# Performance work log

Measured on AMD Instinct MI355X. Metric: run time of the kernel, lower is better.

The kernel has to match this reference:

```python
import jax, jax.numpy as jnp
import numpy as np

BATCH, SEQ, DIM = 4, 4096, 256
DT_RANK, D_STATE, NUM_TOKENS = 16, 16, 1024


def _adapool(x, T):
    # uniform window mean == AdaptiveAvgPool1d when S % T == 0
    B, S, D = x.shape
    return x.reshape(B, T, S // T, D).mean(axis=2)


def _layernorm(x, g, b, eps=1e-5):
    mu = x.mean(-1, keepdims=True)
    var = ((x - mu) ** 2).mean(-1, keepdims=True)
    return (x - mu) * jax.lax.rsqrt(var + eps) * g + b


def _gauss_mask(T):
    c = (T + 1) // 2
    idx = jnp.arange(T, dtype=jnp.float32)
    sigma = jnp.abs(idx - c).mean()
    w = jnp.exp(-0.5 * (idx - c) ** 2 / sigma ** 2)
    return w / w.sum()


def _ssm(x, Wdbc, Wdt, bdt, Alog, D):
    A = -jnp.exp(Alog)                                     # (Dm, N)
    dbc = x @ Wdbc.T                                       # (B,L,dt+2N)
    delta = jax.nn.softplus(dbc[..., :DT_RANK] @ Wdt.T + bdt)   # (B,L,Dm)
    Bm = dbc[..., DT_RANK:DT_RANK + D_STATE]               # (B,L,N)
    Cm = dbc[..., DT_RANK + D_STATE:]                      # (B,L,N)
    deltaA = jnp.exp(delta[..., None] * A)                 # (B,L,Dm,N)
    BX = (delta[..., None] * Bm[:, :, None, :]) * x[..., None]
    def comb(c1, c2):
        a1, x1 = c1
        a2, x2 = c2
        return (a2 * a1, a2 * x1 + x2)
    _, hs = jax.lax.associative_scan(comb, (deltaA, BX), axis=1)
    y = jnp.einsum('bldn,bln->bld', hs, Cm) + D * x
    return y


def setup_inputs():
    key = jax.random.key(0)
    ks = jax.random.split(key, 16)
    s = 0.05
    Alog = jnp.tile(jnp.log(jnp.arange(1.0, D_STATE + 1.0, dtype=jnp.float32))[None, :], (DIM, 1))
    return {
        'x': jax.random.normal(ks[0], (BATCH, SEQ, DIM), jnp.float32),
        'ln_g': jnp.ones((DIM,), jnp.float32),
        'ln_b': jnp.zeros((DIM,), jnp.float32),
        'W1': jax.random.normal(ks[1], (DIM, DIM), jnp.float32) * s,
        'b1': jnp.zeros((DIM,), jnp.float32),
        'W2': jax.random.normal(ks[2], (DIM, DIM), jnp.float32) * s,
        'b2': jnp.zeros((DIM,), jnp.float32),
        'Wcf': jax.random.normal(ks[3], (DIM, DIM), jnp.float32) * s,
        'bcf': jnp.zeros((DIM,), jnp.float32),
        'Wcb': jax.random.normal(ks[4], (DIM, DIM), jnp.float32) * s,
        'bcb': jnp.zeros((DIM,), jnp.float32),
        'Wdbc_f': jax.random.normal(ks[5], (DT_RANK + 2 * D_STATE, DIM), jnp.float32) * s,
        'Wdt_f': jax.random.normal(ks[6], (DIM, DT_RANK), jnp.float32) * s,
        'bdt_f': jnp.zeros((DIM,), jnp.float32),
        'Alog_f': Alog,
        'D_f': jnp.ones((DIM,), jnp.float32),
        'Wdbc_b': jax.random.normal(ks[7], (DT_RANK + 2 * D_STATE, DIM), jnp.float32) * s,
        'Wdt_b': jax.random.normal(ks[8], (DIM, DT_RANK), jnp.float32) * s,
        'bdt_b': jnp.zeros((DIM,), jnp.float32),
        'Alog_b': Alog,
        'D_b': jnp.ones((DIM,), jnp.float32),
    }


def reference(x, ln_g, ln_b, W1, b1, W2, b2, Wcf, bcf, Wcb, bcb,
              Wdbc_f, Wdt_f, bdt_f, Alog_f, D_f,
              Wdbc_b, Wdt_b, bdt_b, Alog_b, D_b):
    skip = _adapool(x, NUM_TOKENS)
    xn = _layernorm(x, ln_g, ln_b)
    z = xn @ W1.T + b1
    xp = xn @ W2.T + b2
    mask = _gauss_mask(NUM_TOKENS)[None, :, None]

    # forward direction: 1x1 conv (= channel linear) -> softplus -> SSM
    h1 = jax.nn.softplus(jnp.einsum('bsd,ed->bse', xp, Wcf) + bcf)
    x1 = _ssm(h1, Wdbc_f, Wdt_f, bdt_f, Alog_f, D_f)
    x1 = jax.nn.silu(_adapool(x1, NUM_TOKENS) * mask)

    # backward direction on flipped sequence
    h2 = jax.nn.softplus(jnp.einsum('bsd,ed->bse', xp[:, ::-1], Wcb) + bcb)
    x2 = _ssm(h2, Wdbc_b, Wdt_b, bdt_b, Alog_b, D_b)[:, ::-1]
    x2 = jax.nn.silu(_adapool(x2, NUM_TOKENS) * mask)

    zp = jax.nn.silu(_adapool(z, NUM_TOKENS))
    return zp * x1 + zp * x2 + skip
```

## Files before the change

kernel.cpp:

```cpp
#include <hip/hip_runtime.h>
#include <math.h>


namespace {
constexpr int BB = 4;
constexpr int LL = 4096;
constexpr int DD = 256;
constexpr int NS = 16;
constexpr int NCH = 64;
constexpr int CLEN = 64;
constexpr int TOK = 1024;

constexpr size_t NROW = (size_t)BB * LL;
constexpr size_t NE   = NROW * DD;
constexpr size_t NP   = (size_t)BB * TOK * DD;
constexpr size_t NBC  = NROW * NS;
constexpr size_t NAGG = 2ull * BB * DD * NCH * NS;

constexpr size_t O_H1X  = 0;
constexpr size_t O_G2X  = NE / 2;
constexpr size_t O_H1T  = NE;
constexpr size_t O_G2T  = NE + NE / 2;
constexpr size_t O_DLTF = 2 * NE;
constexpr size_t O_XN   = O_DLTF;
constexpr size_t O_DLTB = 2 * NE + NE / 2;
constexpr size_t O_BMF  = 3 * NE;
constexpr size_t O_CMF  = O_BMF + NBC / 2;
constexpr size_t O_BMB  = O_CMF + NBC / 2;
constexpr size_t O_CMB  = O_BMB + NBC / 2;
constexpr size_t O_ZP   = O_CMB + NBC / 2;
constexpr size_t O_SKIP = O_ZP + NP;
constexpr size_t O_Y1   = O_SKIP + NP;
constexpr size_t O_Y2   = O_Y1 + NP;
constexpr size_t O_WF1  = O_Y2 + NP;
constexpr size_t O_BF1  = O_WF1 + 768 * 256 / 2;
constexpr size_t O_WF2F = O_BF1 + 768;
constexpr size_t O_B2F  = O_WF2F + 384 * 256 / 2;
constexpr size_t O_WF2B = O_B2F + 384;
constexpr size_t O_B2B  = O_WF2B + 384 * 256 / 2;
constexpr size_t O_APROD = O_B2B + 384;
constexpr size_t O_HEND = O_APROD + NAGG;
constexpr size_t O_HIN  = O_HEND + NAGG;
constexpr size_t O_MASK = O_HIN + NAGG;

constexpr int SST = 136;
}

typedef __bf16 bf16x8 __attribute__((ext_vector_type(8)));
typedef __bf16 bf16x4 __attribute__((ext_vector_type(4)));
typedef float f32x4 __attribute__((ext_vector_type(4)));

__device__ __forceinline__ float softplusf(float x) {
    return fmaxf(x, 0.f) + __logf(1.f + __expf(-fabsf(x)));
}
__device__ __forceinline__ float siluf(float x) {
    return x / (1.f + __expf(-x));
}
__device__ __forceinline__ void gl_lds16(const void* g, void* l) {
    __builtin_amdgcn_global_load_lds((const __attribute__((address_space(1))) unsigned int*)g,
                                     (__attribute__((address_space(3))) unsigned int*)l, 16, 0, 0);
}
__device__ __forceinline__ int st_addr(int col, int row) {
    return col * SST + ((((row >> 3) ^ (col >> 3)) & 15) << 3) + (row & 7);
}
__device__ __forceinline__ void pow_chain(float e1, float* p) {
    p[0] = e1;
    p[1] = e1 * e1;
    p[2] = p[1] * e1;
    p[3] = p[1] * p[1];
    p[4] = p[3] * p[0];
    p[5] = p[3] * p[1];
    p[6] = p[3] * p[2];
    p[7] = p[3] * p[3];
    p[8]  = p[7] * p[0];
    p[9]  = p[7] * p[1];
    p[10] = p[7] * p[2];
    p[11] = p[7] * p[3];
    p[12] = p[7] * p[4];
    p[13] = p[7] * p[5];
    p[14] = p[7] * p[6];
    p[15] = p[7] * p[7];
}

__global__ __launch_bounds__(256) void prep_all_kernel(
    const float* __restrict__ W1, const float* __restrict__ b1,
    const float* __restrict__ W2, const float* __restrict__ b2,
    const float* __restrict__ Wcf, const float* __restrict__ bcf,
    const float* __restrict__ Wcb, const float* __restrict__ bcb,
    const float* __restrict__ Wdt_f, const float* __restrict__ Wdbc_f, const float* __restrict__ bdt_f,
    const float* __restrict__ Wdt_b, const float* __restrict__ Wdbc_b, const float* __restrict__ bdt_b,
    __bf16* __restrict__ Wf1, float* __restrict__ bf1,
    __bf16* __restrict__ Wf2f, float* __restrict__ b2f,
    __bf16* __restrict__ Wf2b, float* __restrict__ b2b,
    float* __restrict__ mask)
{
    int bx = blockIdx.x, mat = blockIdx.y, k = threadIdx.x;
    if (bx < 256) {
        int j = bx;
        const float* Wc = mat ? Wcb : Wcf;
        float acc = 0.f, accb = 0.f;
#pragma unroll 8
        for (int m = 0; m < 256; ++m) {
            float w = Wc[j * 256 + m];
            acc  = fmaf(w, W2[m * 256 + k], acc);
            accb = fmaf(w, b2[m], accb);
        }
        Wf1[(size_t)(256 + mat * 256 + j) * 256 + k] = (__bf16)acc;
        if (k == 0) bf1[256 + mat * 256 + j] = accb + (mat ? bcb[j] : bcf[j]);
        if (mat == 0) {
            Wf1[(size_t)j * 256 + k] = (__bf16)W1[j * 256 + k];
            if (k == 0) bf1[j] = b1[j];
        }
    } else if (bx < 640) {
        int j = bx - 256;
        const float* Wdt  = mat ? Wdt_b : Wdt_f;
        const float* Wdbc = mat ? Wdbc_b : Wdbc_f;
        const float* bdt  = mat ? bdt_b : bdt_f;
        __bf16* Wf2 = mat ? Wf2b : Wf2f;
        float* b2x  = mat ? b2b : b2f;
        float val;
        if (j < 256) {
            float acc = 0.f;
#pragma unroll
            for (int m = 0; m < 16; ++m)
                acc = fmaf(Wdt[j * 16 + m], Wdbc[m * 256 + k], acc);
            val = acc;
        } else if (j < 288) {
            val = Wdbc[(16 + (j - 256)) * 256 + k];
        } else {
            val = 0.f;
        }
        Wf2[(size_t)j * 256 + k] = (__bf16)val;
        if (k == 0) b2x[j] = (j < 256) ? bdt[j] : 0.f;
    } else if (mat == 0) {
        __shared__ float red[4];
        __shared__ float sb;
        float w[4];
        float loc = 0.f;
#pragma unroll
        for (int q = 0; q < 4; ++q) {
            float dd = (float)(k + 256 * q) - 512.f;
            w[q] = __expf(-0.5f * dd * dd * (1.f / 65536.f));
            loc += w[q];
        }
        for (int o = 32; o > 0; o >>= 1) loc += __shfl_xor(loc, o, 64);
        if ((k & 63) == 0) red[k >> 6] = loc;
        __syncthreads();
        if (k == 0) sb = red[0] + red[1] + red[2] + red[3];
        __syncthreads();
        float inv = 1.f / sb;
#pragma unroll
        for (int q = 0; q < 4; ++q) mask[k + 256 * q] = w[q] * inv;
    }
}

__global__ __launch_bounds__(256) void ln_kernel(
    const float* __restrict__ x, const float* __restrict__ lng, const float* __restrict__ lnb,
    __bf16* __restrict__ xn, float* __restrict__ skipo)
{
    __shared__ float red[32];
    __shared__ float mv[8];
    int t = threadIdx.x;
    int r0 = blockIdx.x * 4;
    float gg = lng[t], bbv = lnb[t];
    float v[4], s[4], q[4];
#pragma unroll
    for (int i = 0; i < 4; ++i) {
        v[i] = x[(size_t)(r0 + i) * 256 + t];
        s[i] = v[i];
        q[i] = v[i] * v[i];
    }
    for (int o = 32; o > 0; o >>= 1) {
#pragma unroll
        for (int i = 0; i < 4; ++i) {
            s[i] += __shfl_xor(s[i], o, 64);
            q[i] += __shfl_xor(q[i], o, 64);
        }
    }
    if ((t & 63) == 0) {
        int w = t >> 6;
#pragma unroll
        for (int i = 0; i < 4; ++i) { red[i * 4 + w] = s[i]; red[16 + i * 4 + w] = q[i]; }
    }
    __syncthreads();
    if (t < 4) {
        float S = red[t * 4 + 0] + red[t * 4 + 1] + red[t * 4 + 2] + red[t * 4 + 3];
        float Q = red[16 + t * 4 + 0] + red[16 + t * 4 + 1] + red[16 + t * 4 + 2] + red[16 + t * 4 + 3];
        float mu = S * (1.f / 256.f);
        mv[t * 2] = mu;
        mv[t * 2 + 1] = rsqrtf(Q * (1.f / 256.f) - mu * mu + 1e-5f);
    }
    __syncthreads();
    float acc = 0.f;
#pragma unroll
    for (int i = 0; i < 4; ++i) {
        xn[(size_t)(r0 + i) * 256 + t] = (__bf16)((v[i] - mv[i * 2]) * mv[i * 2 + 1] * gg + bbv);
        acc += v[i];
    }
    int b = r0 >> 12;
    int g = (r0 & 4095) >> 2;
    skipo[((size_t)b * TOK + g) * 256 + t] = acc * 0.25f;
}

__global__ __launch_bounds__(256) void gemm1_mfma(
    const __bf16* __restrict__ A, const __bf16* __restrict__ Bw, const float* __restrict__ bias,
    float* __restrict__ zp, __bf16* __restrict__ h1x, __bf16* __restrict__ g2x,
    __bf16* __restrict__ h1T, __bf16* __restrict__ g2T)
{
    __shared__ __align__(16) __bf16 SH[128 * SST];
    __bf16* As = SH;
    __bf16* Bs = SH + 4096;
    int tid = threadIdx.x;
    int lane = tid & 63, wv = tid >> 6;
    int wr = wv >> 1, wc = wv & 1;
    int lm = lane & 15, lq = lane >> 4;
    int m0 = blockIdx.x << 7, n0 = blockIdx.y << 7;

    const __bf16* ga0 = A  + (size_t)(m0 + wv * 32 + lm) * 256 + lq * 8;
    const __bf16* ga1 = ga0 + 16 * 256;
    const __bf16* gb0 = Bw + (size_t)(n0 + wv * 32 + lm) * 256 + lq * 8;
    const __bf16* gb1 = gb0 + 16 * 256;
    __bf16* la0 = &As[(wv * 2    ) * 512];
    __bf16* la1 = &As[(wv * 2 + 1) * 512];
    __bf16* lb0 = &Bs[(wv * 2    ) * 512];
    __bf16* lb1 = &Bs[(wv * 2 + 1) * 512];

    f32x4 acc[4][4];
#pragma unroll
    for (int i = 0; i < 4; ++i)
#pragma unroll
        for (int j = 0; j < 4; ++j) acc[i][j] = 0;

    for (int k0 = 0; k0 < 256; k0 += 32) {
        __syncthreads();
        gl_lds16(ga0 + k0, la0);
        gl_lds16(ga1 + k0, la1);
        gl_lds16(gb0 + k0, lb0);
        gl_lds16(gb1 + k0, lb1);
        __syncthreads();
        bf16x8 af[4], bfr[4];
#pragma unroll
        for (int i = 0; i < 4; ++i)
            af[i] = *(const bf16x8*)&As[(wr * 4 + i) * 512 + lane * 8];
#pragma unroll
        for (int j = 0; j < 4; ++j)
            bfr[j] = *(const bf16x8*)&Bs[(wc * 4 + j) * 512 + lane * 8];
#pragma unroll
        for (int i = 0; i < 4; ++i)
#pragma unroll
            for (int j = 0; j < 4; ++j)
                acc[i][j] = __builtin_amdgcn_mfma_f32_16x16x32_bf16(af[i], bfr[j], acc[i][j], 0, 0, 0);
    }

    int target = blockIdx.y >> 1;
    int colbase = (blockIdx.y & 1) * 128;
    __syncthreads();
    if (target == 0) {
        float* zs = (float*)SH;
#pragma unroll
        for (int j = 0; j < 4; ++j) {
            int coll = wc * 64 + j * 16 + lm;
            float bv = bias[n0 + coll];
#pragma unroll
            for (int i = 0; i < 4; ++i) {
                int gl = wr * 16 + i * 4 + lq;
                float s = acc[i][j][0] + acc[i][j][1] + acc[i][j][2] + acc[i][j][3];
                zs[gl * 132 + coll] = siluf(0.25f * s + bv);
            }
        }
        __syncthreads();
        int b = m0 >> 12, g0 = (m0 & 4095) >> 2;
        int rl = tid >> 5;
        int c4 = (tid & 31) * 4;
#pragma unroll
        for (int p = 0; p < 4; ++p) {
            int g = p * 8 + rl;
            float4 v = *(float4*)&zs[g * 132 + c4];
            *(float4*)&zp[((size_t)b * TOK + g0 + g) * 256 + colbase + c4] = v;
        }
    } else {
        __bf16* hs = SH;
#pragma unroll
        for (int j = 0; j < 4; ++j) {
            int coll = wc * 64 + j * 16 + lm;
            float bv = bias[n0 + coll];
#pragma unroll
            for (int i = 0; i < 4; ++i) {
                int rl = wr * 64 + i * 16 + lq * 4;
                bf16x4 v4;
#pragma unroll
                for (int r = 0; r < 4; ++r)
                    v4[r] = (__bf16)softplusf(acc[i][j][r] + bv);
                *(bf16x4*)&hs[st_addr(coll, rl)] = v4;
            }
        }
        __syncthreads();
        __bf16* outp = (target == 1) ? h1x : g2x;
        __bf16* outT = (target == 1) ? h1T : g2T;
        {
            int tg = tid & 15;
#pragma unroll
            for (int it = 0; it < 8; ++it) {
                int dl_ = it * 16 + (tid >> 4);
                bf16x8 v = *(const bf16x8*)&hs[dl_ * SST + (((tg ^ (dl_ >> 3)) & 15) << 3)];
                *(bf16x8*)&outT[(size_t)(colbase + dl_) * 16384 + m0 + tg * 8] = v;
            }
        }
        {
            int rl2 = tid >> 4;
            int c8 = (tid & 15) * 8;
#pragma unroll
            for (int p = 0; p < 8; ++p) {
                int row = p * 16 + rl2;
                bf16x8 v;
#pragma unroll
                for (int e = 0; e < 8; ++e) v[e] = hs[st_addr(c8 + e, row)];
                *(bf16x8*)&outp[(size_t)(m0 + row) * 256 + colbase + c8] = v;
            }
        }
    }
}

__global__ __launch_bounds__(256) void gemm2_mfma(
    const __bf16* __restrict__ h1x, const __bf16* __restrict__ g2x,
    const __bf16* __restrict__ Wf, const float* __restrict__ bf2,
    const __bf16* __restrict__ Wb, const float* __restrict__ bb2,
    __bf16* __restrict__ dTf, __bf16* __restrict__ dTb,
    __bf16* __restrict__ BmF, __bf16* __restrict__ CmF,
    __bf16* __restrict__ BmB, __bf16* __restrict__ CmB)
{
    __shared__ __align__(16) __bf16 SH[128 * SST];
    __bf16* As = SH;
    __bf16* Bs = SH + 4096;
    int tid = threadIdx.x;
    int lane = tid & 63, wv = tid >> 6;
    int wr = wv >> 1, wc = wv & 1;
    int lm = lane & 15, lq = lane >> 4;
    int m0 = blockIdx.x << 7, n0 = blockIdx.y << 7;
    int dir = blockIdx.z;
    const __bf16* A    = dir ? g2x : h1x;
    const __bf16* Bw   = dir ? Wb : Wf;
    const float* bias  = dir ? bb2 : bf2;
    __bf16* dT = dir ? dTb : dTf;
    __bf16* Bm = dir ? BmB : BmF;
    __bf16* Cm = dir ? CmB : CmF;

    const __bf16* ga0 = A  + (size_t)(m0 + wv * 32 + lm) * 256 + lq * 8;
    const __bf16* ga1 = ga0 + 16 * 256;
    const __bf16* gb0 = Bw + (size_t)(n0 + wv * 32 + lm) * 256 + lq * 8;
    const __bf16* gb1 = gb0 + 16 * 256;
    __bf16* la0 = &As[(wv * 2    ) * 512];
    __bf16* la1 = &As[(wv * 2 + 1) * 512];
    __bf16* lb0 = &Bs[(wv * 2    ) * 512];
    __bf16* lb1 = &Bs[(wv * 2 + 1) * 512];

    f32x4 acc[4][4];
#pragma unroll
    for (int i = 0; i < 4; ++i)
#pragma unroll
        for (int j = 0; j < 4; ++j) acc[i][j] = 0;

    for (int k0 = 0; k0 < 256; k0 += 32) {
        __syncthreads();
        gl_lds16(ga0 + k0, la0);
        gl_lds16(ga1 + k0, la1);
        gl_lds16(gb0 + k0, lb0);
        gl_lds16(gb1 + k0, lb1);
        __syncthreads();
        bf16x8 af[4], bfr[4];
#pragma unroll
        for (int i = 0; i < 4; ++i)
            af[i] = *(const bf16x8*)&As[(wr * 4 + i) * 512 + lane * 8];
#pragma unroll
        for (int j = 0; j < 4; ++j)
            bfr[j] = *(const bf16x8*)&Bs[(wc * 4 + j) * 512 + lane * 8];
#pragma unroll
        for (int i = 0; i < 4; ++i)
#pragma unroll
            for (int j = 0; j < 4; ++j)
                acc[i][j] = __builtin_amdgcn_mfma_f32_16x16x32_bf16(af[i], bfr[j], acc[i][j], 0, 0, 0);
    }

    __syncthreads();
    if (blockIdx.y < 2) {
        __bf16* hs = SH;
        int colbase = blockIdx.y * 128;
#pragma unroll
        for (int j = 0; j < 4; ++j) {
            int coll = wc * 64 + j * 16 + lm;
            float bv = bias[n0 + coll];
#pragma unroll
            for (int i = 0; i < 4; ++i) {
                int rl = wr * 64 + i * 16 + lq * 4;
                bf16x4 v4;
#pragma unroll
                for (int r = 0; r < 4; ++r)
                    v4[r] = (__bf16)softplusf(acc[i][j][r] + bv);
                *(bf16x4*)&hs[st_addr(coll, rl)] = v4;
            }
        }
        __syncthreads();
        int tg = tid & 15;
#pragma unroll
        for (int it = 0; it < 8; ++it) {
            int dl_ = it * 16 + (tid >> 4);
            bf16x8 v = *(const bf16x8*)&hs[dl_ * SST + (((tg ^ (dl_ >> 3)) & 15) << 3)];
            *(bf16x8*)&dT[(size_t)(colbase + dl_) * 16384 + m0 + tg * 8] = v;
        }
    } else {
        __bf16* bs_ = SH;
        __bf16* cs_ = SH + 128 * 24;
        if (wc == 0) {
#pragma unroll
            for (int j = 0; j < 2; ++j) {
                int coll = j * 16 + lm;
                float bv = bias[n0 + coll];
                __bf16* dst = j ? cs_ : bs_;
#pragma unroll
                for (int i = 0; i < 4; ++i) {
                    int rl = wr * 64 + i * 16 + lq * 4;
#pragma unroll
                    for (int r = 0; r < 4; ++r)
                        dst[(rl + r) * 24 + lm] = (__bf16)(acc[i][j][r] + bv);
                }
            }
        }
        __syncthreads();
        int row = tid >> 1;
        int c8 = (tid & 1) * 8;
        bf16x8 vb = *(bf16x8*)&bs_[row * 24 + c8];
        bf16x8 vc = *(bf16x8*)&cs_[row * 24 + c8];
        *(bf16x8*)&Bm[(size_t)(m0 + row) * 16 + c8] = vb;
        *(bf16x8*)&Cm[(size_t)(m0 + row) * 16 + c8] = vc;
    }
}

__global__ __launch_bounds__(256) void scan1_kernel(
    const __bf16* __restrict__ dTf, const __bf16* __restrict__ dTb,
    const __bf16* __restrict__ xTf, const __bf16* __restrict__ xTb,
    const __bf16* __restrict__ bmf, const __bf16* __restrict__ bmb,
    const float* __restrict__ alogf, const float* __restrict__ alogb,
    float* __restrict__ aprod, float* __restrict__ hend)
{
    int d = threadIdx.x;
    int c = blockIdx.x, b = blockIdx.y, dir = blockIdx.z;
    const __bf16* dT = dir ? dTb : dTf;
    const __bf16* xT = dir ? xTb : xTf;
    const __bf16* Bm = dir ? bmb : bmf;
    const float* Alog = dir ? alogb : alogf;

    float A[16];
    bool intOK = true;
#pragma unroll
    for (int n = 0; n < 16; ++n) {
        A[n] = -__expf(Alog[(size_t)d * 16 + n]);
        intOK = intOK && (fabsf(A[n] + (float)(n + 1)) < 1e-3f);
    }
    float h[16];
#pragma unroll
    for (int n = 0; n < 16; ++n) h[n] = 0.f;
    float sd = 0.f;
    size_t tb = (size_t)d * 16384 + (size_t)b * 4096 + (size_t)c * CLEN;
    size_t rowb = (size_t)b * LL + (size_t)c * CLEN;
    if (intOK) {
        for (int g = 0; g < 8; ++g) {
            int tblk = dir ? (56 - 8 * g) : 8 * g;
            bf16x8 dv = *(const bf16x8*)&dT[tb + tblk];
            bf16x8 xv8 = *(const bf16x8*)&xT[tb + tblk];
#pragma unroll
            for (int ii = 0; ii < 8; ++ii) {
                int i = dir ? (7 - ii) : ii;
                float dlt = (float)dv[i];
                float xv  = (float)xv8[i];
                float common = dlt * xv;
                sd += dlt;
                float p[16];
                pow_chain(__expf(-dlt), p);
                const bf16x8* Bp = (const bf16x8*)&Bm[(rowb + tblk + i) * NS];
                bf16x8 b0 = Bp[0], b1 = Bp[1];
#pragma unroll
                for (int n = 0; n < 8; ++n) {
                    h[n]     = fmaf(p[n],     h[n],     common * (float)b0[n]);
                    h[n + 8] = fmaf(p[n + 8], h[n + 8], common * (float)b1[n]);
                }
            }
        }
        float pe[16];
        pow_chain(__expf(-sd), pe);
        size_t idx = ((((size_t)dir * BB + b) * DD + d) * NCH + c) * NS;
#pragma unroll
        for (int q = 0; q < 4; ++q) {
            float4 av, hv;
            av.x = pe[q * 4 + 0]; av.y = pe[q * 4 + 1]; av.z = pe[q * 4 + 2]; av.w = pe[q * 4 + 3];
            hv.x = h[q * 4 + 0];  hv.y = h[q * 4 + 1];  hv.z = h[q * 4 + 2];  hv.w = h[q * 4 + 3];
            *(float4*)&aprod[idx + q * 4] = av;
            *(float4*)&hend[idx + q * 4] = hv;
        }
    } else {
        for (int g = 0; g < 8; ++g) {
            int tblk = dir ? (56 - 8 * g) : 8 * g;
            bf16x8 dv = *(const bf16x8*)&dT[tb + tblk];
            bf16x8 xv8 = *(const bf16x8*)&xT[tb + tblk];
#pragma unroll
            for (int ii = 0; ii < 8; ++ii) {
                int i = dir ? (7 - ii) : ii;
                float dlt = (float)dv[i];
                float xv  = (float)xv8[i];
                float common = dlt * xv;
                sd += dlt;
                const bf16x8* Bp = (const bf16x8*)&Bm[(rowb + tblk + i) * NS];
                bf16x8 b0 = Bp[0], b1 = Bp[1];
#pragma unroll
                for (int n = 0; n < 8; ++n) {
                    h[n]     = fmaf(__expf(dlt * A[n]),     h[n],     common * (float)b0[n]);
                    h[n + 8] = fmaf(__expf(dlt * A[n + 8]), h[n + 8], common * (float)b1[n]);
                }
            }
        }
        size_t idx = ((((size_t)dir * BB + b) * DD + d) * NCH + c) * NS;
#pragma unroll
        for (int n = 0; n < 16; ++n) {
            aprod[idx + n] = __expf(sd * A[n]);
            hend[idx + n] = h[n];
        }
    }
}

__global__ __launch_bounds__(256) void scan2_kernel(
    const float* __restrict__ aprod, const float* __restrict__ hend,
    float* __restrict__ hin)
{
    int g = blockIdx.x * 256 + threadIdx.x;
    int n = g & 15, d = (g >> 4) & 255, b = (g >> 12) & 3, dir = (g >> 14) & 1;
    size_t bidx = (((size_t)dir * BB + b) * DD + d) * NCH;
    float s = 0.f;
    if (!dir) {
#pragma unroll 8
        for (int c = 0; c < NCH; ++c) {
            size_t idx = (bidx + c) * NS + n;
            hin[idx] = s;
            s = fmaf(aprod[idx], s, hend[idx]);
        }
    } else {
#pragma unroll 8
        for (int c = NCH - 1; c >= 0; --c) {
            size_t idx = (bidx + c) * NS + n;
            hin[idx] = s;
            s = fmaf(aprod[idx], s, hend[idx]);
        }
    }
}

__global__ __launch_bounds__(256) void scan3_kernel(
    const __bf16* __restrict__ dTf, const __bf16* __restrict__ dTb,
    const __bf16* __restrict__ xTf, const __bf16* __restrict__ xTb,
    const __bf16* __restrict__ bmf, const __bf16* __restrict__ bmb,
    const __bf16* __restrict__ cmf, const __bf16* __restrict__ cmb,
    const float* __restrict__ alogf, const float* __restrict__ alogb,
    const float* __restrict__ Dfp, const float* __restrict__ Dbp,
    const float* __restrict__ hin,
    float* __restrict__ y1, float* __restrict__ y2)
{
    int d = threadIdx.x;
    int c = blockIdx.x, b = blockIdx.y, dir = blockIdx.z;
    const __bf16* dT = dir ? dTb : dTf;
    const __bf16* xT = dir ? xTb : xTf;
    const __bf16* Bm = dir ? bmb : bmf;
    const __bf16* Cm = dir ? cmb : cmf;
    const float* Alog = dir ? alogb : alogf;
    const float* Dv   = dir ? Dbp : Dfp;
    float* yout = dir ? y2 : y1;

    float A[16];
    bool intOK = true;
#pragma unroll
    for (int n = 0; n < 16; ++n) {
        A[n] = -__expf(Alog[(size_t)d * 16 + n]);
        intOK = intOK && (fabsf(A[n] + (float)(n + 1)) < 1e-3f);
    }
    float Dd = Dv[d];
    float h[16];
    size_t idx = ((((size_t)dir * BB + b) * DD + d) * NCH + c) * NS;
#pragma unroll
    for (int q = 0; q < 4; ++q) {
        float4 hv = *(const float4*)&hin[idx + q * 4];
        h[q * 4 + 0] = hv.x; h[q * 4 + 1] = hv.y; h[q * 4 + 2] = hv.z; h[q * 4 + 3] = hv.w;
    }
    size_t tb = (size_t)d * 16384 + (size_t)b * 4096 + (size_t)c * CLEN;
    size_t rowb = (size_t)b * LL + (size_t)c * CLEN;
    int base = c * CLEN;
    float pool = 0.f;
    if (intOK) {
        for (int g = 0; g < 8; ++g) {
            int tblk = dir ? (56 - 8 * g) : 8 * g;
            bf16x8 dv = *(const bf16x8*)&dT[tb + tblk];
            bf16x8 xv8 = *(const bf16x8*)&xT[tb + tblk];
#pragma unroll
            for (int ii = 0; ii < 8; ++ii) {
                int i = dir ? (7 - ii) : ii;
                float dlt = (float)dv[i];
                float xv  = (float)xv8[i];
                float common = dlt * xv;
                float p[16];
                pow_chain(__expf(-dlt), p);
                const bf16x8* Bp = (const bf16x8*)&Bm[(rowb + tblk + i) * NS];
                const bf16x8* Cp = (const bf16x8*)&Cm[(rowb + tblk + i) * NS];
                bf16x8 b0 = Bp[0], b1 = Bp[1];
                bf16x8 c0 = Cp[0], c1 = Cp[1];
                float yac = 0.f;
#pragma unroll
                for (int n = 0; n < 8; ++n) {
                    h[n]     = fmaf(p[n],     h[n],     common * (float)b0[n]);
                    h[n + 8] = fmaf(p[n + 8], h[n + 8], common * (float)b1[n]);
                    yac = fmaf(h[n], (float)c0[n], yac);
                    yac = fmaf(h[n + 8], (float)c1[n], yac);
                }
                pool += yac + Dd * xv;
                int t = base + tblk + i;
                bool gend = dir ? ((t & 3) == 0) : ((t & 3) == 3);
                if (gend) {
                    yout[((size_t)b * TOK + (t >> 2)) * DD + d] = pool * 0.25f;
                    pool = 0.f;
                }
            }
        }
    } else {
        for (int g = 0; g < 8; ++g) {
            int tblk = dir ? (56 - 8 * g) : 8 * g;
            bf16x8 dv = *(const bf16x8*)&dT[tb + tblk];
            bf16x8 xv8 = *(const bf16x8*)&xT[tb + tblk];
#pragma unroll
            for (int ii = 0; ii < 8; ++ii) {
                int i = dir ? (7 - ii) : ii;
                float dlt = (float)dv[i];
                float xv  = (float)xv8[i];
                float common = dlt * xv;
                const bf16x8* Bp = (const bf16x8*)&Bm[(rowb + tblk + i) * NS];
                const bf16x8* Cp = (const bf16x8*)&Cm[(rowb + tblk + i) * NS];
                bf16x8 b0 = Bp[0], b1 = Bp[1];
                bf16x8 c0 = Cp[0], c1 = Cp[1];
                float yac = 0.f;
#pragma unroll
                for (int n = 0; n < 8; ++n) {
                    h[n]     = fmaf(__expf(dlt * A[n]),     h[n],     common * (float)b0[n]);
                    h[n + 8] = fmaf(__expf(dlt * A[n + 8]), h[n + 8], common * (float)b1[n]);
                    yac = fmaf(h[n], (float)c0[n], yac);
                    yac = fmaf(h[n + 8], (float)c1[n], yac);
                }
                pool += yac + Dd * xv;
                int t = base + tblk + i;
                bool gend = dir ? ((t & 3) == 0) : ((t & 3) == 3);
                if (gend) {
                    yout[((size_t)b * TOK + (t >> 2)) * DD + d] = pool * 0.25f;
                    pool = 0.f;
                }
            }
        }
    }
}

__global__ __launch_bounds__(256) void final_kernel(
    const float* __restrict__ zp, const float* __restrict__ y1, const float* __restrict__ y2,
    const float* __restrict__ mask, const float* __restrict__ skipi, float* __restrict__ out)
{
    int p = blockIdx.x;
    int g = p & 1023;
    int d = threadIdx.x;
    size_t ip = (size_t)p * 256 + d;
    float mk = mask[g];
    float a1 = y1[ip] * mk, a2 = y2[ip] * mk;
    out[ip] = zp[ip] * (siluf(a1) + siluf(a2)) + skipi[ip];
}

extern "C" void kernel_launch(void* const* d_in, const int* in_sizes, int n_in,
                              void* d_out, int out_size, void* d_ws, size_t ws_size,
                              hipStream_t stream)
{
    const float* x      = (const float*)d_in[0];
    const float* ln_g   = (const float*)d_in[1];
    const float* ln_b   = (const float*)d_in[2];
    const float* W1     = (const float*)d_in[3];
    const float* b1     = (const float*)d_in[4];
    const float* W2     = (const float*)d_in[5];
    const float* b2     = (const float*)d_in[6];
    const float* Wcf    = (const float*)d_in[7];
    const float* bcf    = (const float*)d_in[8];
    const float* Wcb    = (const float*)d_in[9];
    const float* bcb    = (const float*)d_in[10];
    const float* Wdbc_f = (const float*)d_in[11];
    const float* Wdt_f  = (const float*)d_in[12];
    const float* bdt_f  = (const float*)d_in[13];
    const float* Alog_f = (const float*)d_in[14];
    const float* D_f    = (const float*)d_in[15];
    const float* Wdbc_b = (const float*)d_in[16];
    const float* Wdt_b  = (const float*)d_in[17];
    const float* bdt_b  = (const float*)d_in[18];
    const float* Alog_b = (const float*)d_in[19];
    const float* D_b    = (const float*)d_in[20];
    float* out = (float*)d_out;
    float* ws  = (float*)d_ws;

    __bf16* h1x = (__bf16*)(ws + O_H1X);
    __bf16* g2x = (__bf16*)(ws + O_G2X);
    __bf16* h1T = (__bf16*)(ws + O_H1T);
    __bf16* g2T = (__bf16*)(ws + O_G2T);
    __bf16* xnb = (__bf16*)(ws + O_XN);
    __bf16* dTf = (__bf16*)(ws + O_DLTF);
    __bf16* dTb = (__bf16*)(ws + O_DLTB);
    __bf16* bmf = (__bf16*)(ws + O_BMF);
    __bf16* cmf = (__bf16*)(ws + O_CMF);
    __bf16* bmb = (__bf16*)(ws + O_BMB);
    __bf16* cmb = (__bf16*)(ws + O_CMB);
    float* zpb  = ws + O_ZP;
    float* skb  = ws + O_SKIP;
    float* y1b  = ws + O_Y1;
    float* y2b  = ws + O_Y2;
    __bf16* wf1 = (__bf16*)(ws + O_WF1);
    float* bf1  = ws + O_BF1;
    __bf16* wf2f = (__bf16*)(ws + O_WF2F);
    float* b2f  = ws + O_B2F;
    __bf16* wf2b = (__bf16*)(ws + O_WF2B);
    float* b2b  = ws + O_B2B;
    float* apr  = ws + O_APROD;
    float* hnd  = ws + O_HEND;
    float* hin  = ws + O_HIN;
    float* mkb  = ws + O_MASK;

    prep_all_kernel<<<dim3(641, 2), 256, 0, stream>>>(
        W1, b1, W2, b2, Wcf, bcf, Wcb, bcb,
        Wdt_f, Wdbc_f, bdt_f, Wdt_b, Wdbc_b, bdt_b,
        wf1, bf1, wf2f, b2f, wf2b, b2b, mkb);
    ln_kernel<<<4096, 256, 0, stream>>>(x, ln_g, ln_b, xnb, skb);
    gemm1_mfma<<<dim3(128, 6), 256, 0, stream>>>(xnb, wf1, bf1, zpb, h1x, g2x, h1T, g2T);
    gemm2_mfma<<<dim3(128, 3, 2), 256, 0, stream>>>(h1x, g2x, wf2f, b2f, wf2b, b2b,
                                                    dTf, dTb, bmf, cmf, bmb, cmb);
    scan1_kernel<<<dim3(NCH, BB, 2), 256, 0, stream>>>(dTf, dTb, h1T, g2T, bmf, bmb,
                                                       Alog_f, Alog_b, apr, hnd);
    scan2_kernel<<<128, 256, 0, stream>>>(apr, hnd, hin);
    scan3_kernel<<<dim3(NCH, BB, 2), 256, 0, stream>>>(dTf, dTb, h1T, g2T, bmf, bmb, cmf, cmb,
                                                       Alog_f, Alog_b, D_f, D_b, hin, y1b, y2b);
    final_kernel<<<4096, 256, 0, stream>>>(zpb, y1b, y2b, mkb, skb, out);
}
```

Measured before the change: 249.9 us.

## Interleave transposed delta/x in 8-step groups and store chunk sums instead of decay products

Changes the transposed delta and activation buffers from a per-channel contiguous layout (stride 16384) to groups of 8 timesteps interleaved across channels. Adjacent threads in the scan kernels now read adjacent 16-byte vectors, which coalesces those loads. The chunk summaries become [chunk][n][d] with d innermost, and scan1 stores only the summed delta per chunk rather than 16 decay products. scan2 recomputes exp(sd*A) from that sum, cutting summary traffic at the cost of extra exp work in the small serial pass.

```diff
diff --git a/kernel.cpp b/kernel.cpp
--- a/kernel.cpp
+++ b/kernel.cpp
@@ -16,6 +16,7 @@
 constexpr size_t NP   = (size_t)BB * TOK * DD;
 constexpr size_t NBC  = NROW * NS;
 constexpr size_t NAGG = 2ull * BB * DD * NCH * NS;
+constexpr size_t NSD  = 2ull * BB * NCH * DD;
 
 constexpr size_t O_H1X  = 0;
 constexpr size_t O_G2X  = NE / 2;
@@ -38,8 +39,8 @@
 constexpr size_t O_B2F  = O_WF2F + 384 * 256 / 2;
 constexpr size_t O_WF2B = O_B2F + 384;
 constexpr size_t O_B2B  = O_WF2B + 384 * 256 / 2;
-constexpr size_t O_APROD = O_B2B + 384;
-constexpr size_t O_HEND = O_APROD + NAGG;
+constexpr size_t O_SD   = O_B2B + 384;
+constexpr size_t O_HEND = O_SD + NSD;
 constexpr size_t O_HIN  = O_HEND + NAGG;
 constexpr size_t O_MASK = O_HIN + NAGG;
 
@@ -298,12 +299,12 @@
         __bf16* outp = (target == 1) ? h1x : g2x;
         __bf16* outT = (target == 1) ? h1T : g2T;
         {
-            int tg = tid & 15;
+            int tg = tid >> 4;
 #pragma unroll
             for (int it = 0; it < 8; ++it) {
-                int dl_ = it * 16 + (tid >> 4);
-                bf16x8 v = *(const bf16x8*)&hs[dl_ * SST + (((tg ^ (dl_ >> 3)) & 15) << 3)];
-                *(bf16x8*)&outT[(size_t)(colbase + dl_) * 16384 + m0 + tg * 8] = v;
+                int dcol = it * 16 + (tid & 15);
+                bf16x8 v = *(const bf16x8*)&hs[dcol * SST + (((tg ^ (dcol >> 3)) & 15) << 3)];
+                *(bf16x8*)&outT[(((size_t)(m0 >> 3) + tg) * 256 + colbase + dcol) * 8] = v;
             }
         }
         {
@@ -400,12 +401,12 @@
             }
         }
         __syncthreads();
-        int tg = tid & 15;
+        int tg = tid >> 4;
 #pragma unroll
         for (int it = 0; it < 8; ++it) {
-            int dl_ = it * 16 + (tid >> 4);
-            bf16x8 v = *(const bf16x8*)&hs[dl_ * SST + (((tg ^ (dl_ >> 3)) & 15) << 3)];
-            *(bf16x8*)&dT[(size_t)(colbase + dl_) * 16384 + m0 + tg * 8] = v;
+            int dcol = it * 16 + (tid & 15);
+            bf16x8 v = *(const bf16x8*)&hs[dcol * SST + (((tg ^ (dcol >> 3)) & 15) << 3)];
+            *(bf16x8*)&dT[(((size_t)(m0 >> 3) + tg) * 256 + colbase + dcol) * 8] = v;
         }
     } else {
         __bf16* bs_ = SH;
@@ -440,7 +441,7 @@
     const __bf16* __restrict__ xTf, const __bf16* __restrict__ xTb,
     const __bf16* __restrict__ bmf, const __bf16* __restrict__ bmb,
     const float* __restrict__ alogf, const float* __restrict__ alogb,
-    float* __restrict__ aprod, float* __restrict__ hend)
+    float* __restrict__ sdb, float* __restrict__ hend)
 {
     int d = threadIdx.x;
     int c = blockIdx.x, b = blockIdx.y, dir = blockIdx.z;
@@ -460,13 +461,14 @@
 #pragma unroll
     for (int n = 0; n < 16; ++n) h[n] = 0.f;
     float sd = 0.f;
-    size_t tb = (size_t)d * 16384 + (size_t)b * 4096 + (size_t)c * CLEN;
+    size_t rg0 = (size_t)b * 512 + (size_t)c * 8;
     size_t rowb = (size_t)b * LL + (size_t)c * CLEN;
     if (intOK) {
         for (int g = 0; g < 8; ++g) {
-            int tblk = dir ? (56 - 8 * g) : 8 * g;
-            bf16x8 dv = *(const bf16x8*)&dT[tb + tblk];
-            bf16x8 xv8 = *(const bf16x8*)&xT[tb + tblk];
+            int gg = dir ? (7 - g) : g;
+            size_t ti = ((rg0 + gg) * 256 + d) * 8;
+            bf16x8 dv = *(const bf16x8*)&dT[ti];
+            bf16x8 xv8 = *(const bf16x8*)&xT[ti];
 #pragma unroll
             for (int ii = 0; ii < 8; ++ii) {
                 int i = dir ? (7 - ii) : ii;
@@ -476,7 +478,7 @@
                 sd += dlt;
                 float p[16];
                 pow_chain(__expf(-dlt), p);
-                const bf16x8* Bp = (const bf16x8*)&Bm[(rowb + tblk + i) * NS];
+                const bf16x8* Bp = (const bf16x8*)&Bm[(rowb + gg * 8 + i) * NS];
                 bf16x8 b0 = Bp[0], b1 = Bp[1];
 #pragma unroll
                 for (int n = 0; n < 8; ++n) {
@@ -485,22 +487,12 @@
                 }
             }
         }
-        float pe[16];
-        pow_chain(__expf(-sd), pe);
-        size_t idx = ((((size_t)dir * BB + b) * DD + d) * NCH + c) * NS;
-#pragma unroll
-        for (int q = 0; q < 4; ++q) {
-            float4 av, hv;
-            av.x = pe[q * 4 + 0]; av.y = pe[q * 4 + 1]; av.z = pe[q * 4 + 2]; av.w = pe[q * 4 + 3];
-            hv.x = h[q * 4 + 0];  hv.y = h[q * 4 + 1];  hv.z = h[q * 4 + 2];  hv.w = h[q * 4 + 3];
-            *(float4*)&aprod[idx + q * 4] = av;
-            *(float4*)&hend[idx + q * 4] = hv;
-        }
     } else {
         for (int g = 0; g < 8; ++g) {
-            int tblk = dir ? (56 - 8 * g) : 8 * g;
-            bf16x8 dv = *(const bf16x8*)&dT[tb + tblk];
-            bf16x8 xv8 = *(const bf16x8*)&xT[tb + tblk];
+            int gg = dir ? (7 - g) : g;
+            size_t ti = ((rg0 + gg) * 256 + d) * 8;
+            bf16x8 dv = *(const bf16x8*)&dT[ti];
+            bf16x8 xv8 = *(const bf16x8*)&xT[ti];
 #pragma unroll
             for (int ii = 0; ii < 8; ++ii) {
                 int i = dir ? (7 - ii) : ii;
@@ -508,7 +500,7 @@
                 float xv  = (float)xv8[i];
                 float common = dlt * xv;
                 sd += dlt;
-                const bf16x8* Bp = (const bf16x8*)&Bm[(rowb + tblk + i) * NS];
+                const bf16x8* Bp = (const bf16x8*)&Bm[(rowb + gg * 8 + i) * NS];
                 bf16x8 b0 = Bp[0], b1 = Bp[1];
 #pragma unroll
                 for (int n = 0; n < 8; ++n) {
@@ -517,36 +509,43 @@
                 }
             }
         }
-        size_t idx = ((((size_t)dir * BB + b) * DD + d) * NCH + c) * NS;
-#pragma unroll
-        for (int n = 0; n < 16; ++n) {
-            aprod[idx + n] = __expf(sd * A[n]);
-            hend[idx + n] = h[n];
-        }
-    }
+    }
+    size_t sbase = (size_t)(dir * 4 + b) * NCH + c;
+    sdb[sbase * 256 + d] = sd;
+    size_t hb = sbase * 16 * 256 + d;
+#pragma unroll
+    for (int n = 0; n < 16; ++n) hend[hb + (size_t)n * 256] = h[n];
 }
 
 __global__ __launch_bounds__(256) void scan2_kernel(
-    const float* __restrict__ aprod, const float* __restrict__ hend,
+    const float* __restrict__ sdb, const float* __restrict__ hend,
+    const float* __restrict__ alogf, const float* __restrict__ alogb,
     float* __restrict__ hin)
 {
-    int g = blockIdx.x * 256 + threadIdx.x;
-    int n = g & 15, d = (g >> 4) & 255, b = (g >> 12) & 3, dir = (g >> 14) & 1;
-    size_t bidx = (((size_t)dir * BB + b) * DD + d) * NCH;
+    int blk = blockIdx.x;
+    int n = blk & 15, b = (blk >> 4) & 3, dir = blk >> 6;
+    int d = threadIdx.x;
+    const float* Alog = dir ? alogb : alogf;
+    float A_dn = -__expf(Alog[(size_t)d * 16 + n]);
+    size_t basec = (size_t)(dir * 4 + b) * NCH;
     float s = 0.f;
     if (!dir) {
 #pragma unroll 8
         for (int c = 0; c < NCH; ++c) {
-            size_t idx = (bidx + c) * NS + n;
+            float sdv = sdb[(basec + c) * 256 + d];
+            size_t idx = ((basec + c) * 16 + n) * 256 + d;
+            float he = hend[idx];
             hin[idx] = s;
-            s = fmaf(aprod[idx], s, hend[idx]);
+            s = fmaf(__expf(sdv * A_dn), s, he);
         }
     } else {
 #pragma unroll 8
         for (int c = NCH - 1; c >= 0; --c) {
-            size_t idx = (bidx + c) * NS + n;
+            float sdv = sdb[(basec + c) * 256 + d];
+            size_t idx = ((basec + c) * 16 + n) * 256 + d;
+            float he = hend[idx];
             hin[idx] = s;
-            s = fmaf(aprod[idx], s, hend[idx]);
+            s = fmaf(__expf(sdv * A_dn), s, he);
         }
     }
 }
@@ -580,21 +579,20 @@
     }
     float Dd = Dv[d];
     float h[16];
-    size_t idx = ((((size_t)dir * BB + b) * DD + d) * NCH + c) * NS;
-#pragma unroll
-    for (int q = 0; q < 4; ++q) {
-        float4 hv = *(const float4*)&hin[idx + q * 4];
-        h[q * 4 + 0] = hv.x; h[q * 4 + 1] = hv.y; h[q * 4 + 2] = hv.z; h[q * 4 + 3] = hv.w;
-    }
-    size_t tb = (size_t)d * 16384 + (size_t)b * 4096 + (size_t)c * CLEN;
+    size_t hb = ((size_t)(dir * 4 + b) * NCH + c) * 16 * 256 + d;
+#pragma unroll
+    for (int n = 0; n < 16; ++n) h[n] = hin[hb + (size_t)n * 256];
+
+    size_t rg0 = (size_t)b * 512 + (size_t)c * 8;
     size_t rowb = (size_t)b * LL + (size_t)c * CLEN;
     int base = c * CLEN;
     float pool = 0.f;
     if (intOK) {
         for (int g = 0; g < 8; ++g) {
-            int tblk = dir ? (56 - 8 * g) : 8 * g;
-            bf16x8 dv = *(const bf16x8*)&dT[tb + tblk];
-            bf16x8 xv8 = *(const bf16x8*)&xT[tb + tblk];
+            int gg = dir ? (7 - g) : g;
+            size_t ti = ((rg0 + gg) * 256 + d) * 8;
+            bf16x8 dv = *(const bf16x8*)&dT[ti];
+            bf16x8 xv8 = *(const bf16x8*)&xT[ti];
 #pragma unroll
             for (int ii = 0; ii < 8; ++ii) {
                 int i = dir ? (7 - ii) : ii;
@@ -603,8 +601,9 @@
                 float common = dlt * xv;
                 float p[16];
                 pow_chain(__expf(-dlt), p);
-                const bf16x8* Bp = (const bf16x8*)&Bm[(rowb + tblk + i) * NS];
-                const bf16x8* Cp = (const bf16x8*)&Cm[(rowb + tblk + i) * NS];
+                size_t row = rowb + gg * 8 + i;
+                const bf16x8* Bp = (const bf16x8*)&Bm[row * NS];
+                const bf16x8* Cp = (const bf16x8*)&Cm[row * NS];
                 bf16x8 b0 = Bp[0], b1 = Bp[1];
                 bf16x8 c0 = Cp[0], c1 = Cp[1];
                 float yac = 0.f;
@@ -616,7 +615,7 @@
                     yac = fmaf(h[n + 8], (float)c1[n], yac);
                 }
                 pool += yac + Dd * xv;
-                int t = base + tblk + i;
+                int t = base + gg * 8 + i;
                 bool gend = dir ? ((t & 3) == 0) : ((t & 3) == 3);
                 if (gend) {
                     yout[((size_t)b * TOK + (t >> 2)) * DD + d] = pool * 0.25f;
@@ -626,17 +625,19 @@
         }
     } else {
         for (int g = 0; g < 8; ++g) {
-            int tblk = dir ? (56 - 8 * g) : 8 * g;
-            bf16x8 dv = *(const bf16x8*)&dT[tb + tblk];
-            bf16x8 xv8 = *(const bf16x8*)&xT[tb + tblk];
+            int gg = dir ? (7 - g) : g;
+            size_t ti = ((rg0 + gg) * 256 + d) * 8;
+            bf16x8 dv = *(const bf16x8*)&dT[ti];
+            bf16x8 xv8 = *(const bf16x8*)&xT[ti];
 #pragma unroll
             for (int ii = 0; ii < 8; ++ii) {
                 int i = dir ? (7 - ii) : ii;
                 float dlt = (float)dv[i];
                 float xv  = (float)xv8[i];
                 float common = dlt * xv;
-                const bf16x8* Bp = (const bf16x8*)&Bm[(rowb + tblk + i) * NS];
-                const bf16x8* Cp = (const bf16x8*)&Cm[(rowb + tblk + i) * NS];
+                size_t row = rowb + gg * 8 + i;
+                const bf16x8* Bp = (const bf16x8*)&Bm[row * NS];
+                const bf16x8* Cp = (const bf16x8*)&Cm[row * NS];
                 bf16x8 b0 = Bp[0], b1 = Bp[1];
                 bf16x8 c0 = Cp[0], c1 = Cp[1];
                 float yac = 0.f;
@@ -648,7 +649,7 @@
                     yac = fmaf(h[n + 8], (float)c1[n], yac);
                 }
                 pool += yac + Dd * xv;
-                int t = base + tblk + i;
+                int t = base + gg * 8 + i;
                 bool gend = dir ? ((t & 3) == 0) : ((t & 3) == 3);
                 if (gend) {
                     yout[((size_t)b * TOK + (t >> 2)) * DD + d] = pool * 0.25f;
@@ -721,7 +722,7 @@
     float* b2f  = ws + O_B2F;
     __bf16* wf2b = (__bf16*)(ws + O_WF2B);
     float* b2b  = ws + O_B2B;
-    float* apr  = ws + O_APROD;
+    float* sdb  = ws + O_SD;
     float* hnd  = ws + O_HEND;
     float* hin  = ws + O_HIN;
     float* mkb  = ws + O_MASK;
@@ -735,8 +736,8 @@
     gemm2_mfma<<<dim3(128, 3, 2), 256, 0, stream>>>(h1x, g2x, wf2f, b2f, wf2b, b2b,
                                                     dTf, dTb, bmf, cmf, bmb, cmb);
     scan1_kernel<<<dim3(NCH, BB, 2), 256, 0, stream>>>(dTf, dTb, h1T, g2T, bmf, bmb,
-                                                       Alog_f, Alog_b, apr, hnd);
-    scan2_kernel<<<128, 256, 0, stream>>>(apr, hnd, hin);
+                                                       Alog_f, Alog_b, sdb, hnd);
+    scan2_kernel<<<128, 256, 0, stream>>>(sdb, hnd, Alog_f, Alog_b, hin);
     scan3_kernel<<<dim3(NCH, BB, 2), 256, 0, stream>>>(dTf, dTb, h1T, g2T, bmf, bmb, cmf, cmb,
                                                        Alog_f, Alog_b, D_f, D_b, hin, y1b, y2b);
     final_kernel<<<4096, 256, 0, stream>>>(zpb, y1b, y2b, mkb, skb, out);
```

Result: faster. 230.2 us (-7.9%).
